# Kernel tuning notes

Hardware: AMD Instinct MI355X
Metric: run time of the kernel (lower is better)

## Reference

```python
import jax, jax.numpy as jnp
import numpy as np

DIM = 2048
DIM_HEAD = 128
HEADS = 16
FF_MULT = 4
ATTN_INNER = DIM_HEAD * HEADS          # 2048
FF_INNER = DIM * FF_MULT               # 8192
FUSED = ATTN_INNER + DIM_HEAD + DIM_HEAD + 2 * FF_INNER  # 18688


def setup_inputs() -> dict:
    key = jax.random.key(0)
    k1, k2, k3, k4 = jax.random.split(key, 4)
    B, N = 2, 2048
    x = jax.random.normal(k1, (B, N, DIM), dtype=jnp.float32)
    gamma = jnp.ones((DIM,), dtype=jnp.float32)
    w_fused = jax.random.normal(k2, (DIM, FUSED), dtype=jnp.float32) * 0.02
    w_attn_out = jax.random.normal(k3, (ATTN_INNER, DIM), dtype=jnp.float32) * 0.02
    w_ff_out = jax.random.normal(k4, (FF_INNER, DIM), dtype=jnp.float32) * 0.02
    return {"x": x, "gamma": gamma, "w_fused": w_fused,
            "w_attn_out": w_attn_out, "w_ff_out": w_ff_out}


def _rotate_half(t):
    d = t.shape[-1] // 2
    x1, x2 = t[..., :d], t[..., d:]
    return jnp.concatenate((-x2, x1), axis=-1)


def _apply_rope(pos, t):
    return t * jnp.cos(pos) + _rotate_half(t) * jnp.sin(pos)


def reference(x, gamma, w_fused, w_attn_out, w_ff_out):
    B, N, _ = x.shape
    # LayerNorm (beta fixed at zero)
    mu = jnp.mean(x, axis=-1, keepdims=True)
    var = jnp.var(x, axis=-1, keepdims=True)
    xn = (x - mu) / jnp.sqrt(var + 1e-5) * gamma

    proj = xn @ w_fused  # [B, N, FUSED]
    q = proj[..., :ATTN_INNER]
    k = proj[..., ATTN_INNER:ATTN_INNER + DIM_HEAD]
    v = proj[..., ATTN_INNER + DIM_HEAD:ATTN_INNER + 2 * DIM_HEAD]
    ff = proj[..., ATTN_INNER + 2 * DIM_HEAD:]

    q = q.reshape(B, N, HEADS, DIM_HEAD).transpose(0, 2, 1, 3)  # b h n d

    # rotary positions: [N, DIM_HEAD]
    inv_freq = 1.0 / (10000.0 ** (jnp.arange(0, DIM_HEAD, 2, dtype=jnp.float32) / DIM_HEAD))
    freqs = jnp.arange(N, dtype=jnp.float32)[:, None] * inv_freq[None, :]
    pos = jnp.concatenate((freqs, freqs), axis=-1)

    q = _apply_rope(pos, q)
    k = _apply_rope(pos, k)
    q = q * (DIM_HEAD ** -0.5)

    sim = jnp.einsum('bhid,bjd->bhij', q, k)  # multi-query: shared k head
    neg = -jnp.finfo(sim.dtype).max
    causal = jnp.triu(jnp.ones((N, N), dtype=bool), 1)
    sim = jnp.where(causal, neg, sim)
    sim = sim - jax.lax.stop_gradient(jnp.max(sim, axis=-1, keepdims=True))
    attn = jax.nn.softmax(sim, axis=-1)
    out = jnp.einsum('bhij,bjd->bhid', attn, v)
    out = out.transpose(0, 2, 1, 3).reshape(B, N, ATTN_INNER)

    # SwiGLU feedforward
    ff_x, gate = ff[..., :FF_INNER], ff[..., FF_INNER:]
    ff_out = (jax.nn.silu(gate) * ff_x) @ w_ff_out

    return out @ w_attn_out + ff_out
```

## Files before the change

kernel.cpp:

```cpp
#include <hip/hip_runtime.h>
#include <hip/hip_bf16.h>

typedef __attribute__((ext_vector_type(4))) float f32x4;
typedef __attribute__((ext_vector_type(8))) __bf16 bf16x8;

#define DIMC 2048
#define NSEQ 2048
#define BATCH 2
#define HEADSC 16
#define DHEAD 128
#define ATTN_IN 2048
#define FF_IN 8192
#define FUSED_COLS 18688
#define ROWS 4096
#define KCAT 10240

constexpr size_t OFF_XN   = 0;
constexpr size_t OFF_Q    = 16777216;
constexpr size_t OFF_K    = 33554432;
constexpr size_t OFF_VT   = 34603008;
constexpr size_t OFF_ACAT = 35651584;
constexpr size_t OFF_GATE = 119537664;
constexpr size_t OFF_WFT  = 186646528;
constexpr size_t OFF_WCT  = 263192576;

__global__ __launch_bounds__(256) void ln_kernel(const float* __restrict__ x,
                                                 const float* __restrict__ gamma,
                                                 __hip_bfloat16* __restrict__ xn) {
  int row = blockIdx.x;
  int tid = threadIdx.x;
  int lane = tid & 63, wave = tid >> 6;
  const float4* xr = (const float4*)(x + (size_t)row * DIMC);
  float4 a = xr[tid], b = xr[tid + 256];
  float s  = a.x + a.y + a.z + a.w + b.x + b.y + b.z + b.w;
  float ss = a.x*a.x + a.y*a.y + a.z*a.z + a.w*a.w + b.x*b.x + b.y*b.y + b.z*b.z + b.w*b.w;
  #pragma unroll
  for (int o = 32; o; o >>= 1) { s += __shfl_down(s, o); ss += __shfl_down(ss, o); }
  __shared__ float red[8];
  if (lane == 0) { red[wave] = s; red[4 + wave] = ss; }
  __syncthreads();
  s  = red[0] + red[1] + red[2] + red[3];
  ss = red[4] + red[5] + red[6] + red[7];
  float mean = s * (1.f / DIMC);
  float var  = ss * (1.f / DIMC) - mean * mean;
  float rstd = rsqrtf(var + 1e-5f);
  const float4* gp = (const float4*)gamma;
  float4 g1 = gp[tid], g2 = gp[tid + 256];
  __hip_bfloat16* o = xn + (size_t)row * DIMC;
  o[tid*4+0]      = __float2bfloat16((a.x - mean) * rstd * g1.x);
  o[tid*4+1]      = __float2bfloat16((a.y - mean) * rstd * g1.y);
  o[tid*4+2]      = __float2bfloat16((a.z - mean) * rstd * g1.z);
  o[tid*4+3]      = __float2bfloat16((a.w - mean) * rstd * g1.w);
  o[1024+tid*4+0] = __float2bfloat16((b.x - mean) * rstd * g2.x);
  o[1024+tid*4+1] = __float2bfloat16((b.y - mean) * rstd * g2.y);
  o[1024+tid*4+2] = __float2bfloat16((b.z - mean) * rstd * g2.z);
  o[1024+tid*4+3] = __float2bfloat16((b.w - mean) * rstd * g2.w);
}

__global__ __launch_bounds__(256) void transpose_bf16(const float* __restrict__ src,
                                                      __hip_bfloat16* __restrict__ dst,
                                                      int R, int C, int dstStride, int dstOff) {
  __shared__ float tile[32][33];
  int c0 = blockIdx.x * 32, r0 = blockIdx.y * 32;
  int tx = threadIdx.x & 31, ty = threadIdx.x >> 5;
  #pragma unroll
  for (int i = 0; i < 32; i += 8)
    tile[ty + i][tx] = src[(size_t)(r0 + ty + i) * C + c0 + tx];
  __syncthreads();
  #pragma unroll
  for (int i = 0; i < 32; i += 8)
    dst[(size_t)(c0 + ty + i) * dstStride + dstOff + r0 + tx] = __float2bfloat16(tile[tx][ty + i]);
}

struct GemmP {
  const __hip_bfloat16* A;
  const __hip_bfloat16* B;
  int K;
  int kTilesPer;
  int nbx;
  int nmn;
  int cpx;
  float* outF0;
  float* outF1;
  int Nout;
  __hip_bfloat16 *q, *kk, *vT, *acat, *gate;
};

#define LDA_Q(BUFIDX, QM) { \
    const char* slot_ = lds + ((BUFIDX) << 16) + ((QM) << 14); \
    _Pragma("unroll") for (int mi = 0; mi < 4; ++mi) \
    _Pragma("unroll") for (int ks = 0; ks < 2; ++ks) { \
      int row_ = (mi << 5) + (wr << 4) + (lane & 15); \
      int ch_  = (ks << 2) + (lane >> 4); \
      af[mi][ks] = *(const bf16x8*)(slot_ + (row_ << 7) + ((ch_ ^ (row_ & 7)) << 4)); } }

#define LDB_Q(DST, BUFIDX, QN) { \
    const char* slot_ = lds + ((BUFIDX) << 16) + 32768 + ((QN) << 14); \
    _Pragma("unroll") for (int ni = 0; ni < 2; ++ni) \
    _Pragma("unroll") for (int ks = 0; ks < 2; ++ks) { \
      int row_ = (ni << 6) + (wn << 4) + (lane & 15); \
      int ch_  = (ks << 2) + (lane >> 4); \
      DST[ni][ks] = *(const bf16x8*)(slot_ + (row_ << 7) + ((ch_ ^ (row_ & 7)) << 4)); } }

#define DO_MFMA_Q(QM, BSET, QN) \
    __builtin_amdgcn_s_setprio(1); \
    _Pragma("unroll") for (int mi = 0; mi < 4; ++mi) \
    _Pragma("unroll") for (int ni = 0; ni < 2; ++ni) \
    _Pragma("unroll") for (int ks = 0; ks < 2; ++ks) \
      acc[(QM)*4+mi][(QN)*2+ni] = __builtin_amdgcn_mfma_f32_16x16x32_bf16( \
          af[mi][ks], BSET[ni][ks], acc[(QM)*4+mi][(QN)*2+ni], 0, 0, 0); \
    __builtin_amdgcn_s_setprio(0);

#define KTILE_BODY(KT, BUFC) \
    LDB_Q(b0r, BUFC, 0); \
    LDA_Q(BUFC, 0); \
    stage(Bb, (KT) + 1, 1, 0); \
    asm volatile("s_waitcnt lgkmcnt(8)"); \
    __builtin_amdgcn_s_barrier(); \
    asm volatile("s_waitcnt lgkmcnt(0)"); \
    __builtin_amdgcn_sched_barrier(0); \
    DO_MFMA_Q(0, b0r, 0); \
    __builtin_amdgcn_s_barrier(); \
    LDB_Q(b1r, BUFC, 1); \
    stage(Bb, (KT) + 1, 1, 1); \
    __builtin_amdgcn_s_barrier(); \
    asm volatile("s_waitcnt lgkmcnt(0)"); \
    __builtin_amdgcn_sched_barrier(0); \
    DO_MFMA_Q(0, b1r, 1); \
    __builtin_amdgcn_s_barrier(); \
    LDA_Q(BUFC, 1); \
    stage(Ab, (KT) + 2, 0, 0); \
    __builtin_amdgcn_s_barrier(); \
    asm volatile("s_waitcnt lgkmcnt(0)"); \
    __builtin_amdgcn_sched_barrier(0); \
    DO_MFMA_Q(1, b0r, 0); \
    __builtin_amdgcn_s_barrier(); \
    stage(Ab, (KT) + 2, 0, 1); \
    asm volatile("s_waitcnt vmcnt(4)" ::: "memory"); \
    __builtin_amdgcn_sched_barrier(0); \
    __builtin_amdgcn_s_barrier(); \
    DO_MFMA_Q(1, b1r, 1);

template<int EPI>
__global__ __launch_bounds__(512, 2) void gemm256(GemmP p) {
  __shared__ __align__(16) char lds[131072];
  const int tid = threadIdx.x;
  const int lane = tid & 63, wave = tid >> 6;
  const int wr = wave >> 2, wn = wave & 3;

  int l = ((int)blockIdx.x & 7) * p.cpx + ((int)blockIdx.x >> 3);
  int kp = l / p.nmn;
  int r = l - kp * p.nmn;
  int per = 8 * p.nbx;
  int g = r / per;
  int rg = r - g * per;
  int by = (g << 3) + (rg & 7);
  int bx = rg >> 3;
  int m0 = by << 8, n0 = bx << 8;

  const int NT = p.kTilesPer;
  const size_t Kb = (size_t)p.K * 2;
  const size_t koff = (size_t)kp * NT * 128;
  const char* Ab = (const char*)p.A + (size_t)m0 * Kb + koff;
  const char* Bb = (const char*)p.B + (size_t)n0 * Kb + koff;

  auto stage = [&](const char* mbase, int ktTgt, int isB, int h) {
    int ks = ktTgt < NT ? ktTgt : NT - 1;
    char* dst = lds + ((ktTgt & 1) << 16) + (isB << 15) + (h << 14);
    #pragma unroll
    for (int j = 0; j < 2; ++j) {
      int c = (j << 9) + tid;
      int row = c >> 3;
      int gl = ((c & 7) ^ (row & 7)) << 4;
      __builtin_amdgcn_global_load_lds(
        (const __attribute__((address_space(1))) void*)(mbase + (size_t)((h << 7) + row) * Kb + (size_t)ks * 128 + gl),
        (__attribute__((address_space(3))) void*)(dst + (c << 4)), 16, 0, 0);
    }
  };

  bf16x8 af[4][2], b0r[2][2], b1r[2][2];
  f32x4 acc[8][4] = {};

  stage(Ab, 0, 0, 0); stage(Ab, 0, 0, 1);
  stage(Bb, 0, 1, 0); stage(Bb, 0, 1, 1);
  stage(Ab, 1, 0, 0); stage(Ab, 1, 0, 1);
  asm volatile("s_waitcnt vmcnt(4)" ::: "memory");
  __builtin_amdgcn_sched_barrier(0);
  __builtin_amdgcn_s_barrier();

  for (int kt = 0; kt < NT; kt += 2) {
    KTILE_BODY(kt, 0);
    KTILE_BODY(kt + 1, 1);
  }

  asm volatile("s_waitcnt vmcnt(0) lgkmcnt(0)" ::: "memory");

  if constexpr (EPI == 1) {
    #pragma unroll
    for (int mig = 0; mig < 8; ++mig) {
      int rr0 = m0 + (mig << 5) + (wr << 4) + ((lane >> 4) << 2);
      #pragma unroll
      for (int nig = 0; nig < 4; ++nig) {
        int cc = n0 + (nig << 6) + (wn << 4) + (lane & 15);
        #pragma unroll
        for (int rr_ = 0; rr_ < 4; ++rr_) {
          int rr = rr0 + rr_;
          int b = rr >> 11, n = rr & 2047;
          __hip_bfloat16 hv = __float2bfloat16(acc[mig][nig][rr_]);
          if (cc < 2048) {
            int h = cc >> 7, d = cc & 127;
            p.q[((((size_t)b << 4) + h) * NSEQ + n) * DHEAD + d] = hv;
          } else if (cc < 2176) {
            p.kk[(size_t)rr * DHEAD + (cc - 2048)] = hv;
          } else if (cc < 2304) {
            p.vT[(((size_t)b << 7) + (cc - 2176)) * NSEQ + n] = hv;
          } else if (cc < 10496) {
            p.acat[(size_t)rr * KCAT + (cc - 256)] = hv;
          } else {
            p.gate[(size_t)rr * FF_IN + (cc - 10496)] = hv;
          }
        }
      }
    }
  } else {
    float* dst = kp ? p.outF1 : p.outF0;
    #pragma unroll
    for (int mig = 0; mig < 8; ++mig) {
      int rr0 = m0 + (mig << 5) + (wr << 4) + ((lane >> 4) << 2);
      #pragma unroll
      for (int nig = 0; nig < 4; ++nig) {
        int cc = n0 + (nig << 6) + (wn << 4) + (lane & 15);
        #pragma unroll
        for (int rr_ = 0; rr_ < 4; ++rr_)
          dst[(size_t)(rr0 + rr_) * p.Nout + cc] = acc[mig][nig][rr_];
      }
    }
  }
}

__global__ __launch_bounds__(256) void addout_kernel(const float* __restrict__ a,
                                                     const float* __restrict__ b,
                                                     float* __restrict__ o, int n4) {
  int i = blockIdx.x * 256 + threadIdx.x;
  if (i < n4) {
    float4 x = ((const float4*)a)[i], y = ((const float4*)b)[i];
    float4 z; z.x = x.x + y.x; z.y = x.y + y.y; z.z = x.z + y.z; z.w = x.w + y.w;
    ((float4*)o)[i] = z;
  }
}

__global__ __launch_bounds__(256) void rope_kernel(__hip_bfloat16* __restrict__ t,
                                                   int totalRows, float scale) {
  int idx = blockIdx.x * 256 + threadIdx.x;
  if (idx >= totalRows * 64) return;
  int i = idx & 63;
  int row = idx >> 6;
  int n = row & (NSEQ - 1);
  float f = __expf(-(float)i * 0.14391157f);
  float ang = (float)n * f;
  float sv, cv;
  sincosf(ang, &sv, &cv);
  __hip_bfloat16* pp = t + (size_t)row * DHEAD;
  float x1 = __bfloat162float(pp[i]);
  float x2 = __bfloat162float(pp[i + 64]);
  pp[i]      = __float2bfloat16((x1 * cv - x2 * sv) * scale);
  pp[i + 64] = __float2bfloat16((x2 * cv + x1 * sv) * scale);
}

__global__ __launch_bounds__(256, 2) void attn_part_kernel(const __hip_bfloat16* __restrict__ q,
                                                           const __hip_bfloat16* __restrict__ k,
                                                           const __hip_bfloat16* __restrict__ vT,
                                                           __hip_bfloat16* __restrict__ opart,
                                                           float* __restrict__ mpart,
                                                           float* __restrict__ lpart) {
  __shared__ __align__(16) char alds[81920];
  char* Ktile = alds;
  char* Vtile = alds + 32768;
  char* Pb    = alds + 65536;
  const int tid = threadIdx.x;
  int c = 79 - (int)blockIdx.x;
  int bh = blockIdx.y;
  int qt, ch;
  if (c < 8)       { qt = c;                 ch = 0; }
  else if (c < 24) { qt = 8  + ((c - 8) >> 1);  ch = (c - 8) & 1; }
  else if (c < 48) { qt = 16 + (c - 24) / 3;    ch = (c - 24) % 3; }
  else             { qt = 24 + ((c - 48) >> 2); ch = (c - 48) & 3; }
  int slot = bh * 80 + c;
  int b = bh >> 4;
  int lane = tid & 63, wave = tid >> 6;
  int q0 = qt << 6;
  int qrow0 = q0 + (wave << 4);
  const __hip_bfloat16* qbase = q + (size_t)bh * NSEQ * DHEAD;
  const char* kbase = (const char*)(k + (size_t)b * NSEQ * DHEAD);
  const char* vbase = (const char*)(vT + (size_t)b * DHEAD * NSEQ);
  char* Pw = Pb + (wave << 12);

  auto stageK = [&](int j0) {
    const char* kb = kbase + (size_t)j0 * 256;
    #pragma unroll
    for (int it = 0; it < 8; ++it) {
      int s = (it << 8) + tid;
      int row = s >> 4, cch = s & 15;
      int sch = (cch & 8) | ((cch & 7) ^ (row & 7));
      __builtin_amdgcn_global_load_lds(
        (const __attribute__((address_space(1))) void*)(kb + (size_t)row * 256 + (sch << 4)),
        (__attribute__((address_space(3))) void*)(Ktile + (s << 4)), 16, 0, 0);
    }
  };
  auto stageV = [&](int j0) {
    const char* vb = vbase + (size_t)j0 * 2;
    #pragma unroll
    for (int it = 0; it < 8; ++it) {
      int s = (it << 8) + tid;
      int row = s >> 4, cch = s & 15;
      int sch = (cch & 8) | ((cch & 7) ^ (row & 7));
      __builtin_amdgcn_global_load_lds(
        (const __attribute__((address_space(1))) void*)(vb + (size_t)row * (NSEQ * 2) + (sch << 4)),
        (__attribute__((address_space(3))) void*)(Vtile + (s << 4)), 16, 0, 0);
    }
  };

  bf16x8 qf[4];
  #pragma unroll
  for (int ks = 0; ks < 4; ++ks)
    qf[ks] = *(const bf16x8*)(qbase + (size_t)(qrow0 + (lane & 15)) * DHEAD + (ks << 5) + ((lane >> 4) << 3));
  {
    const float SCALE = 0.08838834764831845f;
    float nrow = (float)(qrow0 + (lane & 15));
    #pragma unroll
    for (int ks = 0; ks < 2; ++ks) {
      #pragma unroll
      for (int j = 0; j < 8; ++j) {
        int d = (ks << 5) + ((lane >> 4) << 3) + j;
        float f = __expf(-(float)d * 0.14391157f);
        float sv, cv;
        sincosf(nrow * f, &sv, &cv);
        float x1 = (float)qf[ks][j];
        float x2 = (float)qf[ks + 2][j];
        qf[ks][j]     = (__bf16)((x1 * cv - x2 * sv) * SCALE);
        qf[ks + 2][j] = (__bf16)((x2 * cv + x1 * sv) * SCALE);
      }
    }
  }
  f32x4 o[8] = {};
  float mrow[4] = {-1e30f, -1e30f, -1e30f, -1e30f};
  float lrow[4] = {0.f, 0.f, 0.f, 0.f};
  int nTiles = (q0 + 64 + 127) >> 7;
  int jBeg = ch << 2;
  int jEnd = jBeg + 4 < nTiles ? jBeg + 4 : nTiles;

  stageK(jBeg << 7);
  stageV(jBeg << 7);
  asm volatile("s_waitcnt vmcnt(0)" ::: "memory");
  __builtin_amdgcn_s_barrier();

  for (int j2 = jBeg; j2 < jEnd; ++j2) {
    int j0 = j2 << 7;
    bool more = (j2 + 1 < jEnd);
    f32x4 s[8] = {};
    #pragma unroll
    for (int ks = 0; ks < 4; ++ks) {
      bf16x8 kf2[8];
      #pragma unroll
      for (int nf = 0; nf < 8; ++nf) {
        int row_ = (nf << 4) + (lane & 15);
        int ch_  = (ks << 2) + (lane >> 4);
        int sch  = (ch_ & 8) | ((ch_ & 7) ^ (row_ & 7));
        kf2[nf] = *(const bf16x8*)(Ktile + (row_ << 8) + (sch << 4));
      }
      __builtin_amdgcn_s_setprio(1);
      #pragma unroll
      for (int nf = 0; nf < 8; ++nf)
        s[nf] = __builtin_amdgcn_mfma_f32_16x16x32_bf16(qf[ks], kf2[nf], s[nf], 0, 0, 0);
      __builtin_amdgcn_s_setprio(0);
    }
    __builtin_amdgcn_s_barrier();
    if (more) stageK((j0 + 128));
    if (j0 + 127 > q0) {
      #pragma unroll
      for (int nf = 0; nf < 8; ++nf) {
        int cg = j0 + (nf << 4) + (lane & 15);
        #pragma unroll
        for (int r = 0; r < 4; ++r) {
          int rg = qrow0 + ((lane >> 4) << 2) + r;
          if (cg > rg) s[nf][r] = -1e30f;
        }
      }
    }
    float tm[4] = {-1e30f, -1e30f, -1e30f, -1e30f};
    #pragma unroll
    for (int nf = 0; nf < 8; ++nf)
      #pragma unroll
      for (int r = 0; r < 4; ++r) tm[r] = fmaxf(tm[r], s[nf][r]);
    #pragma unroll
    for (int r = 0; r < 4; ++r) {
      #pragma unroll
      for (int msk = 1; msk < 16; msk <<= 1)
        tm[r] = fmaxf(tm[r], __shfl_xor(tm[r], msk));
    }
    float scl[4], ps[4] = {0.f, 0.f, 0.f, 0.f};
    #pragma unroll
    for (int r = 0; r < 4; ++r) {
      float mn = fmaxf(mrow[r], tm[r]);
      scl[r] = __expf(mrow[r] - mn);
      mrow[r] = mn;
    }
    #pragma unroll
    for (int nf = 0; nf < 8; ++nf) {
      #pragma unroll
      for (int r = 0; r < 4; ++r) {
        float pv = __expf(s[nf][r] - mrow[r]);
        ps[r] += pv;
        int prow = ((lane >> 4) << 2) + r;
        int pcol = (nf << 4) + (lane & 15);
        int pch  = pcol >> 3;
        int psch = (pch & 8) | ((pch & 7) ^ (prow & 7));
        *(__hip_bfloat16*)(Pw + (prow << 8) + (psch << 4) + ((pcol & 7) << 1)) = __float2bfloat16(pv);
      }
    }
    #pragma unroll
    for (int r = 0; r < 4; ++r) {
      #pragma unroll
      for (int msk = 1; msk < 16; msk <<= 1) ps[r] += __shfl_xor(ps[r], msk);
      lrow[r] = lrow[r] * scl[r] + ps[r];
    }
    #pragma unroll
    for (int df = 0; df < 8; ++df)
      #pragma unroll
      for (int r = 0; r < 4; ++r) o[df][r] *= scl[r];
    #pragma unroll
    for (int ks2 = 0; ks2 < 4; ++ks2) {
      int prow = lane & 15;
      int pch  = (ks2 << 2) + (lane >> 4);
      int psch = (pch & 8) | ((pch & 7) ^ (prow & 7));
      bf16x8 pf = *(const bf16x8*)(Pw + (prow << 8) + (psch << 4));
      bf16x8 vf2[8];
      #pragma unroll
      for (int df = 0; df < 8; ++df) {
        int row_ = (df << 4) + (lane & 15);
        int ch_  = (ks2 << 2) + (lane >> 4);
        int sch  = (ch_ & 8) | ((ch_ & 7) ^ (row_ & 7));
        vf2[df] = *(const bf16x8*)(Vtile + (row_ << 8) + (sch << 4));
      }
      __builtin_amdgcn_s_setprio(1);
      #pragma unroll
      for (int df = 0; df < 8; ++df)
        o[df] = __builtin_amdgcn_mfma_f32_16x16x32_bf16(pf, vf2[df], o[df], 0, 0, 0);
      __builtin_amdgcn_s_setprio(0);
    }
    if (more) {
      __builtin_amdgcn_s_barrier();
      stageV(j0 + 128);
      asm volatile("s_waitcnt vmcnt(0)" ::: "memory");
      __builtin_amdgcn_s_barrier();
    }
  }
  size_t rbase = ((size_t)slot << 6) + (wave << 4) + ((lane >> 4) << 2);
  #pragma unroll
  for (int df = 0; df < 8; ++df)
    #pragma unroll
    for (int r = 0; r < 4; ++r)
      opart[(rbase + r) * 128 + (df << 4) + (lane & 15)] = __float2bfloat16(o[df][r]);
  if ((lane & 15) == 0) {
    #pragma unroll
    for (int r = 0; r < 4; ++r) { mpart[rbase + r] = mrow[r]; lpart[rbase + r] = lrow[r]; }
  }
}

__global__ __launch_bounds__(256) void attn_comb_kernel(const __hip_bfloat16* __restrict__ opart,
                                                        const float* __restrict__ mpart,
                                                        const float* __restrict__ lpart,
                                                        __hip_bfloat16* __restrict__ acat) {
  int t = blockIdx.x * 256 + threadIdx.x;
  int dg = t & 15;
  int rg = (t >> 4) & 2047;
  int bh = t >> 15;
  int qt = rg >> 6;
  int nc = (qt + 8) >> 3;
  int S = qt;
  if (qt >= 8)  S += qt - 8;
  if (qt >= 16) S += qt - 16;
  if (qt >= 24) S += qt - 24;
  size_t base = (((size_t)bh * 80 + S) << 6) + (rg & 63);
  float M = -1e30f;
  for (int cc = 0; cc < nc; ++cc) M = fmaxf(M, mpart[base + ((size_t)cc << 6)]);
  float O[8] = {};
  float L = 0.f;
  for (int cc = 0; cc < nc; ++cc) {
    size_t rb = base + ((size_t)cc << 6);
    float w = __expf(mpart[rb] - M);
    L += w * lpart[rb];
    bf16x8 ov = *(const bf16x8*)(opart + rb * 128 + (dg << 3));
    #pragma unroll
    for (int j = 0; j < 8; ++j) O[j] += w * (float)ov[j];
  }
  float invL = 1.f / L;
  int b = bh >> 4, h = bh & 15;
  bf16x8 res;
  #pragma unroll
  for (int j = 0; j < 8; ++j) res[j] = (__bf16)(O[j] * invL);
  *(bf16x8*)(acat + ((size_t)(b * 2048 + rg)) * KCAT + (h << 7) + (dg << 3)) = res;
}

__global__ __launch_bounds__(256) void silu_kernel(__hip_bfloat16* __restrict__ acat,
                                                   const __hip_bfloat16* __restrict__ gate) {
  size_t idx = ((size_t)blockIdx.x * 256 + threadIdx.x) << 3;
  int r = (int)(idx >> 13);
  int j = (int)(idx & 8191);
  bf16x8 g = *(const bf16x8*)(gate + idx);
  size_t ai = (size_t)r * KCAT + 2048 + j;
  bf16x8 fx = *(const bf16x8*)(acat + ai);
  bf16x8 res;
  #pragma unroll
  for (int t = 0; t < 8; ++t) {
    float gf = (float)g[t];
    res[t] = (__bf16)((float)fx[t] * gf / (1.f + __expf(-gf)));
  }
  *(bf16x8*)(acat + ai) = res;
}

extern "C" void kernel_launch(void* const* d_in, const int* in_sizes, int n_in,
                              void* d_out, int out_size, void* d_ws, size_t ws_size,
                              hipStream_t stream) {
  (void)in_sizes; (void)n_in; (void)out_size; (void)ws_size;
  const float* x          = (const float*)d_in[0];
  const float* gamma      = (const float*)d_in[1];
  const float* w_fused    = (const float*)d_in[2];
  const float* w_attn_out = (const float*)d_in[3];
  const float* w_ff_out   = (const float*)d_in[4];
  char* ws = (char*)d_ws;
  __hip_bfloat16* xn    = (__hip_bfloat16*)(ws + OFF_XN);
  __hip_bfloat16* qbuf  = (__hip_bfloat16*)(ws + OFF_Q);
  __hip_bfloat16* kbuf  = (__hip_bfloat16*)(ws + OFF_K);
  __hip_bfloat16* vTbuf = (__hip_bfloat16*)(ws + OFF_VT);
  __hip_bfloat16* acat  = (__hip_bfloat16*)(ws + OFF_ACAT);
  __hip_bfloat16* gateb = (__hip_bfloat16*)(ws + OFF_GATE);
  __hip_bfloat16* wfT   = (__hip_bfloat16*)(ws + OFF_WFT);
  __hip_bfloat16* wcT   = (__hip_bfloat16*)(ws + OFF_WCT);
  float* P0 = (float*)(ws + OFF_XN);
  float* P1 = (float*)(ws + OFF_GATE);
  __hip_bfloat16* oPart = (__hip_bfloat16*)(ws + OFF_WFT);
  float* mPart = (float*)(ws + OFF_XN);
  float* lPart = (float*)(ws + OFF_XN + 1048576);

  transpose_bf16<<<dim3(FUSED_COLS / 32, DIMC / 32), 256, 0, stream>>>(w_fused, wfT, DIMC, FUSED_COLS, DIMC, 0);
  transpose_bf16<<<dim3(DIMC / 32, DIMC / 32), 256, 0, stream>>>(w_attn_out, wcT, ATTN_IN, DIMC, KCAT, 0);
  transpose_bf16<<<dim3(DIMC / 32, FF_IN / 32), 256, 0, stream>>>(w_ff_out, wcT, FF_IN, DIMC, KCAT, ATTN_IN);

  ln_kernel<<<ROWS, 256, 0, stream>>>(x, gamma, xn);

  GemmP g1;
  g1.A = xn; g1.B = wfT; g1.K = DIMC; g1.kTilesPer = DIMC / 64;
  g1.nbx = FUSED_COLS / 256; g1.nmn = (FUSED_COLS / 256) * (ROWS / 256);
  g1.cpx = g1.nmn / 8;
  g1.outF0 = nullptr; g1.outF1 = nullptr; g1.Nout = 0;
  g1.q = qbuf; g1.kk = kbuf; g1.vT = vTbuf; g1.acat = acat; g1.gate = gateb;
  gemm256<1><<<g1.nmn, 512, 0, stream>>>(g1);

  rope_kernel<<<(BATCH * NSEQ * 64) / 256, 256, 0, stream>>>(kbuf, BATCH * NSEQ, 1.0f);

  attn_part_kernel<<<dim3(80, BATCH * HEADSC), 256, 0, stream>>>(qbuf, kbuf, vTbuf, oPart, mPart, lPart);
  attn_comb_kernel<<<(BATCH * HEADSC * NSEQ * DHEAD / 8) / 256, 256, 0, stream>>>(oPart, mPart, lPart, acat);

  silu_kernel<<<(int)(((size_t)ROWS * FF_IN / 8) / 256), 256, 0, stream>>>(acat, gateb);

  GemmP g2;
  g2.A = acat; g2.B = wcT; g2.K = KCAT; g2.kTilesPer = (KCAT / 64) / 2;
  g2.nbx = DIMC / 256; g2.nmn = (DIMC / 256) * (ROWS / 256);
  g2.cpx = (g2.nmn * 2) / 8;
  g2.outF0 = P0; g2.outF1 = P1; g2.Nout = DIMC;
  g2.q = nullptr; g2.kk = nullptr; g2.vT = nullptr; g2.acat = nullptr; g2.gate = nullptr;
  gemm256<3><<<g2.nmn * 2, 512, 0, stream>>>(g2);

  addout_kernel<<<(ROWS * DIMC / 4 + 255) / 256, 256, 0, stream>>>(P0, P1, (float*)d_out, ROWS * DIMC / 4);
}
```

Before: 706.9 us.

## Replace quarter-interleaved GEMM k-loop with simple double-buffered loop

Drops the hand-scheduled KTILE_BODY macro, which interleaved quarter-tile global-to-LDS staging, LDS fragment loads and MFMA batches under many barriers and partial waitcnts. Each k-tile now issues all staging for the next tile, reads fragments and runs all MFMAs, then waits for every outstanding global load and syncs once. This cuts the barrier count and simplifies scheduling. In exchange it gives up the two-tile-deep prefetch and the fine-grained overlap, and adds a full vmcnt(0) stall at every tile.

Result: no change. 716.5 us (+1.4%).

```diff
diff --git a/kernel.cpp b/kernel.cpp
--- a/kernel.cpp
+++ b/kernel.cpp
@@ -111,36 +111,6 @@
           af[mi][ks], BSET[ni][ks], acc[(QM)*4+mi][(QN)*2+ni], 0, 0, 0); \
     __builtin_amdgcn_s_setprio(0);
 
-#define KTILE_BODY(KT, BUFC) \
-    LDB_Q(b0r, BUFC, 0); \
-    LDA_Q(BUFC, 0); \
-    stage(Bb, (KT) + 1, 1, 0); \
-    asm volatile("s_waitcnt lgkmcnt(8)"); \
-    __builtin_amdgcn_s_barrier(); \
-    asm volatile("s_waitcnt lgkmcnt(0)"); \
-    __builtin_amdgcn_sched_barrier(0); \
-    DO_MFMA_Q(0, b0r, 0); \
-    __builtin_amdgcn_s_barrier(); \
-    LDB_Q(b1r, BUFC, 1); \
-    stage(Bb, (KT) + 1, 1, 1); \
-    __builtin_amdgcn_s_barrier(); \
-    asm volatile("s_waitcnt lgkmcnt(0)"); \
-    __builtin_amdgcn_sched_barrier(0); \
-    DO_MFMA_Q(0, b1r, 1); \
-    __builtin_amdgcn_s_barrier(); \
-    LDA_Q(BUFC, 1); \
-    stage(Ab, (KT) + 2, 0, 0); \
-    __builtin_amdgcn_s_barrier(); \
-    asm volatile("s_waitcnt lgkmcnt(0)"); \
-    __builtin_amdgcn_sched_barrier(0); \
-    DO_MFMA_Q(1, b0r, 0); \
-    __builtin_amdgcn_s_barrier(); \
-    stage(Ab, (KT) + 2, 0, 1); \
-    asm volatile("s_waitcnt vmcnt(4)" ::: "memory"); \
-    __builtin_amdgcn_sched_barrier(0); \
-    __builtin_amdgcn_s_barrier(); \
-    DO_MFMA_Q(1, b1r, 1);
-
 template<int EPI>
 __global__ __launch_bounds__(512, 2) void gemm256(GemmP p) {
   __shared__ __align__(16) char lds[131072];
@@ -183,14 +153,25 @@
 
   stage(Ab, 0, 0, 0); stage(Ab, 0, 0, 1);
   stage(Bb, 0, 1, 0); stage(Bb, 0, 1, 1);
-  stage(Ab, 1, 0, 0); stage(Ab, 1, 0, 1);
-  asm volatile("s_waitcnt vmcnt(4)" ::: "memory");
+  asm volatile("s_waitcnt vmcnt(0)" ::: "memory");
   __builtin_amdgcn_sched_barrier(0);
   __builtin_amdgcn_s_barrier();
 
-  for (int kt = 0; kt < NT; kt += 2) {
-    KTILE_BODY(kt, 0);
-    KTILE_BODY(kt + 1, 1);
+  for (int kt = 0; kt < NT; ++kt) {
+    const int buf = kt & 1;
+    stage(Ab, kt + 1, 0, 0); stage(Ab, kt + 1, 0, 1);
+    stage(Bb, kt + 1, 1, 0); stage(Bb, kt + 1, 1, 1);
+    LDA_Q(buf, 0);
+    LDB_Q(b0r, buf, 0);
+    LDB_Q(b1r, buf, 1);
+    DO_MFMA_Q(0, b0r, 0);
+    DO_MFMA_Q(0, b1r, 1);
+    LDA_Q(buf, 1);
+    DO_MFMA_Q(1, b0r, 0);
+    DO_MFMA_Q(1, b1r, 1);
+    asm volatile("s_waitcnt vmcnt(0)" ::: "memory");
+    __builtin_amdgcn_sched_barrier(0);
+    __builtin_amdgcn_s_barrier();
   }
 
   asm volatile("s_waitcnt vmcnt(0) lgkmcnt(0)" ::: "memory");
```
